# Kernel optimization log

Hardware: AMD Instinct MI355X
Metric: run time of the kernel (lower is better)

Reference implementation:

```python
import jax, jax.numpy as jnp
import numpy as np

B, T, V, E, H = 4096, 128, 30, 256, 128

def setup_inputs() -> dict:
    key = jax.random.key(0)
    ks = jax.random.split(key, 12)
    inpt = jax.random.randint(ks[0], (B, T), 0, V, dtype=jnp.int32)
    h0 = jax.random.normal(ks[1], (B, H), dtype=jnp.float32)
    c0 = jax.random.normal(ks[2], (B, H), dtype=jnp.float32)
    mask_Y = jnp.ones((B, T), dtype=jnp.float32)
    s_e = 1.0
    s_l = 1.0 / np.sqrt(H)
    s_i = 1.0 / np.sqrt(E)
    emb = jax.random.normal(ks[3], (V, E), dtype=jnp.float32) * s_e
    W_ih = jax.random.normal(ks[4], (4 * H, E), dtype=jnp.float32) * s_i
    b_ih = jax.random.normal(ks[5], (4 * H,), dtype=jnp.float32) * s_i
    W_hh = jax.random.normal(ks[6], (4 * H, H), dtype=jnp.float32) * s_l
    b_hh = jax.random.normal(ks[7], (4 * H,), dtype=jnp.float32) * s_l
    W_lin = jax.random.normal(ks[8], (V, H), dtype=jnp.float32) * s_l
    b_lin = jax.random.normal(ks[9], (V,), dtype=jnp.float32) * s_l
    return {"inpt": inpt, "h0": h0, "c0": c0, "mask_Y": mask_Y, "beta": 1,
            "emb": emb, "W_ih": W_ih, "b_ih": b_ih, "W_hh": W_hh,
            "b_hh": b_hh, "W_lin": W_lin, "b_lin": b_lin}


def reference(inpt, h0, c0, mask_Y, beta, emb, W_ih, b_ih, W_hh, b_hh, W_lin, b_lin):
    # beta == 1 -> teacher forcing every step (u <= beta always), as in source.
    t_max = inpt.shape[1]
    # input tokens fed at steps t=0..t_max-2 are inpt[:, 0:t_max-1]
    x_emb = emb[inpt[:, :t_max - 1]]          # [B, T-1, E]
    xs = (jnp.swapaxes(x_emb, 0, 1),           # [T-1, B, E]
          inpt[:, 1:].T,                       # [T-1, B] true labels
          mask_Y[:, :t_max - 1].T)             # [T-1, B]

    def step(carry, xs_t):
        h, c = carry
        x, y, m = xs_t
        gates = x @ W_ih.T + b_ih + h @ W_hh.T + b_hh   # [B, 4H]
        i, f, g, o = jnp.split(gates, 4, axis=1)
        c2 = jax.nn.sigmoid(f) * c + jax.nn.sigmoid(i) * jnp.tanh(g)
        h2 = jax.nn.sigmoid(o) * jnp.tanh(c2)
        # -log(softmax(logits))[y] == -log_softmax(logits)[y]
        logp = jax.nn.log_softmax(h2 @ W_lin.T + b_lin, axis=1)  # [B, V]
        ce = -jnp.take_along_axis(logp, y[:, None], axis=1)[:, 0]
        return (h2, c2), jnp.sum(ce * m)

    _, step_losses = jax.lax.scan(step, (h0, c0), xs)
    return jnp.sum(step_losses) / jnp.sum(mask_Y)
```

## Files before the change

### kernel.cpp

```cpp
#include <hip/hip_runtime.h>


typedef __bf16 bf16x8 __attribute__((ext_vector_type(8)));
typedef float  f32x4  __attribute__((ext_vector_type(4)));

namespace {
constexpr int Bn = 4096, Tn = 128, Vn = 30, En = 256, Hn = 128, Gn = 512;
constexpr int WS_LOSS  = 0;
constexpr int WS_MASK  = 1;
constexpr int WS_CNT   = 2;
constexpr int WS_XPROJ = 16;
constexpr int WS_WF_F  = WS_XPROJ + Vn * Gn;
}

__device__ __forceinline__ float fexp2(float x) { return __builtin_amdgcn_exp2f(x); }
__device__ __forceinline__ float frcp(float x)  { return __builtin_amdgcn_rcpf(x); }
__device__ __forceinline__ float sigf(float x)  { return frcp(1.f + fexp2(x * -1.44269504f)); }
__device__ __forceinline__ float tanh_(float x) { return 1.f - 2.f * frcp(fexp2(x * 2.88539008f) + 1.f); }

__global__ void k_setup(const float* __restrict__ emb, const float* __restrict__ W_ih,
                        const float* __restrict__ b_ih, const float* __restrict__ b_hh,
                        const float* __restrict__ W_hh, const float* __restrict__ W_lin,
                        float* __restrict__ ws) {
  const int bid = blockIdx.x, tid = threadIdx.x;
  if (bid < 60) {
    __shared__ __align__(16) float es[En];
    int v = bid >> 1;
    int j = ((bid & 1) << 8) + tid;
    es[tid] = emb[v * En + tid];
    __syncthreads();
    float a = b_ih[j] + b_hh[j];
    const float* wr = W_ih + j * En;
#pragma unroll 4
    for (int e = 0; e < En; e += 4) {
      float4 w = *(const float4*)(wr + e);
      float4 x = *(const float4*)(es + e);
      a += x.x * w.x + x.y * w.y + x.z * w.z + x.w * w.w;
    }
    ws[WS_XPROJ + v * Gn + (j & 127) * 4 + (j >> 7)] = a;
  } else if (bid < 92) {
    int fid = (bid - 60) * 256 + tid;
    int l = fid & 63, kt = (fid >> 6) & 3, g = (fid >> 8) & 3, w = fid >> 10;
    int n  = (g * 8 + w) * 16 + (l & 15);
    int k0 = kt * 32 + (l >> 4) * 8;
    const float* src = W_hh + n * Hn + k0;
    union { __bf16 h[8]; uint4 u; } pk;
#pragma unroll
    for (int j = 0; j < 8; ++j) pk.h[j] = (__bf16)src[j];
    __bf16* wf = (__bf16*)(ws + WS_WF_F);
    *(uint4*)(wf + fid * 8) = pk.u;
  } else {
    int fid = (bid - 92) * 256 + tid;
    if (fid < 3) ws[fid] = 0.f;
    int l = fid & 63, kt = (fid >> 6) & 3, n = fid >> 8;
    int col = n * 16 + (l & 15);
    int k0  = kt * 32 + (l >> 4) * 8;
    union { __bf16 h[8]; uint4 u; } pk;
#pragma unroll
    for (int j = 0; j < 8; ++j)
      pk.h[j] = (col < Vn) ? (__bf16)W_lin[col * Hn + k0 + j] : (__bf16)0.f;
    __bf16* wf = (__bf16*)(ws + WS_WF_F);
    *(uint4*)(wf + 65536 + fid * 8) = pk.u;
  }
}

__global__ __launch_bounds__(576, 1) void k_main(
    const int* __restrict__ inpt, const float* __restrict__ h0,
    const float* __restrict__ c0, const float* __restrict__ maskY,
    const float* __restrict__ b_lin, float* __restrict__ ws,
    float* __restrict__ out) {
  __shared__ __align__(16) __bf16 hbuf[2][16][136];
  __shared__ int   tokL[16 * 129];
  __shared__ float maskL[16 * 132];
  __shared__ __align__(16) float logits[16 * 36];
  __shared__ float red[2];

  const float4* X4 = (const float4*)(ws + WS_XPROJ);
  const __bf16* wf = (const __bf16*)(ws + WS_WF_F);
  const __bf16* wlf = wf + 65536;

  const int tid = threadIdx.x;
  const int w = tid >> 6, l = tid & 63, quad = l >> 4, lc = l & 15;
  const int row0 = blockIdx.x * 16;
  const int kh = w * 16 + lc;

  for (int idx = tid; idx < 16 * Tn; idx += 576) {
    int r = idx >> 7, t = idx & 127;
    tokL[r * 129 + t]  = inpt[(row0 + r) * Tn + t];
    maskL[r * 132 + t] = maskY[(row0 + r) * Tn + t];
  }
  for (int idx = tid; idx < 16 * Hn; idx += 576) {
    int r = idx >> 7, k = idx & 127;
    hbuf[0][r][k] = (__bf16)h0[(row0 + r) * Hn + k];
  }

  bf16x8 wreg[4][4];
  float  creg[4];
  float  bias0 = 0.f, bias1 = 0.f, mloc = 0.f;
  if (w < 8) {
#pragma unroll
    for (int g = 0; g < 4; ++g)
#pragma unroll
      for (int kt = 0; kt < 4; ++kt)
        wreg[g][kt] = __builtin_bit_cast(
            bf16x8, *(const uint4*)(wf + (((w * 4 + g) * 4 + kt) * 64 + l) * 8));
#pragma unroll
    for (int p = 0; p < 4; ++p)
      creg[p] = c0[(row0 + quad * 4 + p) * Hn + kh];
    if (w == 7) {
      float s = 0.f;
      const float4* m4 = (const float4*)(maskY + row0 * Tn);
#pragma unroll
      for (int i = 0; i < 8; ++i) s += m4[l + i * 64].x + m4[l + i * 64].y +
                                       m4[l + i * 64].z + m4[l + i * 64].w;
      mloc = s;
    }
  } else {
#pragma unroll
    for (int n = 0; n < 2; ++n)
#pragma unroll
      for (int kt = 0; kt < 4; ++kt)
        wreg[n][kt] = __builtin_bit_cast(
            bf16x8, *(const uint4*)(wlf + ((n * 4 + kt) * 64 + l) * 8));
    bias0 = b_lin[lc];
    bias1 = (lc < Vn - 16) ? b_lin[lc + 16] : -1e30f;
  }
  float ce_acc = 0.f;
  __syncthreads();

  float4 xv[4];
  if (w < 8) {
#pragma unroll
    for (int p = 0; p < 4; ++p)
      xv[p] = X4[tokL[(quad * 4 + p) * 129] * 128 + kh];
  }

  for (int t = 0; t < Tn; ++t) {
    const int par = t & 1;
    const __bf16* hc = &hbuf[par][0][0];
    __bf16*       hn = &hbuf[par ^ 1][0][0];

    if (w < 8) {
      if (t < Tn - 1) {
        bf16x8 af[4];
#pragma unroll
        for (int kt = 0; kt < 4; ++kt)
          af[kt] = __builtin_bit_cast(
              bf16x8, *(const uint4*)(hc + lc * 136 + kt * 32 + quad * 8));

        int tk[4];
#pragma unroll
        for (int p = 0; p < 4; ++p) tk[p] = tokL[(quad * 4 + p) * 129 + t + 1];

        f32x4 acc[4];
#pragma unroll
        for (int p = 0; p < 4; ++p) {
          acc[0][p] = xv[p].x; acc[1][p] = xv[p].y;
          acc[2][p] = xv[p].z; acc[3][p] = xv[p].w;
        }
#pragma unroll
        for (int g = 0; g < 4; ++g)
#pragma unroll
          for (int kt = 0; kt < 4; ++kt)
            acc[g] = __builtin_amdgcn_mfma_f32_16x16x32_bf16(af[kt], wreg[g][kt], acc[g], 0, 0, 0);

        float4 xn[4];
#pragma unroll
        for (int p = 0; p < 4; ++p) xn[p] = X4[tk[p] * 128 + kh];

#pragma unroll
        for (int p = 0; p < 4; ++p) {
          float c2 = sigf(acc[1][p]) * creg[p] + sigf(acc[0][p]) * tanh_(acc[2][p]);
          float h2 = sigf(acc[3][p]) * tanh_(c2);
          creg[p] = c2;
          hn[(quad * 4 + p) * 136 + kh] = (__bf16)h2;
          xv[p] = xn[p];
        }
      }
    } else if (t >= 1) {
      bf16x8 af[4];
#pragma unroll
      for (int kt = 0; kt < 4; ++kt)
        af[kt] = __builtin_bit_cast(
            bf16x8, *(const uint4*)(hc + lc * 136 + kt * 32 + quad * 8));
      f32x4 lacc[2] = {{bias0, bias0, bias0, bias0}, {bias1, bias1, bias1, bias1}};
#pragma unroll
      for (int kt = 0; kt < 4; ++kt) {
        lacc[0] = __builtin_amdgcn_mfma_f32_16x16x32_bf16(af[kt], wreg[0][kt], lacc[0], 0, 0, 0);
        lacc[1] = __builtin_amdgcn_mfma_f32_16x16x32_bf16(af[kt], wreg[1][kt], lacc[1], 0, 0, 0);
      }
#pragma unroll
      for (int p = 0; p < 4; ++p) {
        logits[(quad * 4 + p) * 36 + lc]      = lacc[0][p];
        logits[(quad * 4 + p) * 36 + 16 + lc] = lacc[1][p];
      }
      int row = l >> 2, j = l & 3;
      float4 v0 = *(const float4*)(logits + row * 36 + j * 8);
      float4 v1 = *(const float4*)(logits + row * 36 + j * 8 + 4);
      float m = fmaxf(fmaxf(fmaxf(v0.x, v0.y), fmaxf(v0.z, v0.w)),
                      fmaxf(fmaxf(v1.x, v1.y), fmaxf(v1.z, v1.w)));
      m = fmaxf(m, __shfl_xor(m, 1));
      m = fmaxf(m, __shfl_xor(m, 2));
      float e = fexp2((v0.x - m) * 1.44269504f) + fexp2((v0.y - m) * 1.44269504f) +
                fexp2((v0.z - m) * 1.44269504f) + fexp2((v0.w - m) * 1.44269504f) +
                fexp2((v1.x - m) * 1.44269504f) + fexp2((v1.y - m) * 1.44269504f) +
                fexp2((v1.z - m) * 1.44269504f) + fexp2((v1.w - m) * 1.44269504f);
      e += __shfl_xor(e, 1);
      e += __shfl_xor(e, 2);
      if (j == 0) {
        int   y  = tokL[row * 129 + t];
        float ly = logits[row * 36 + y];
        float ce = (m + __logf(e)) - ly;
        ce_acc += ce * maskL[row * 132 + t - 1];
      }
    }
    __syncthreads();
  }

  if (w == 7) {
#pragma unroll
    for (int off = 32; off > 0; off >>= 1) mloc += __shfl_down(mloc, off);
    if (l == 0) red[0] = mloc;
  }
  __syncthreads();
  if (w == 8) {
#pragma unroll
    for (int off = 32; off > 0; off >>= 1) ce_acc += __shfl_down(ce_acc, off);
    if (l == 0) {
      atomicAdd(ws + WS_LOSS, ce_acc);
      atomicAdd(ws + WS_MASK, red[0]);
      __threadfence();
      unsigned old = atomicAdd((unsigned*)(ws + WS_CNT), 1u);
      if (old == 255) {
        float lv = atomicAdd(ws + WS_LOSS, 0.f);
        float mv = atomicAdd(ws + WS_MASK, 0.f);
        out[0] = lv / mv;
      }
    }
  }
}

extern "C" void kernel_launch(void* const* d_in, const int* in_sizes, int n_in,
                              void* d_out, int out_size, void* d_ws, size_t ws_size,
                              hipStream_t stream) {
  const int*   inpt  = (const int*)  d_in[0];
  const float* h0    = (const float*)d_in[1];
  const float* c0    = (const float*)d_in[2];
  const float* maskY = (const float*)d_in[3];
  const float* emb   = (const float*)d_in[5];
  const float* W_ih  = (const float*)d_in[6];
  const float* b_ih  = (const float*)d_in[7];
  const float* W_hh  = (const float*)d_in[8];
  const float* b_hh  = (const float*)d_in[9];
  const float* W_lin = (const float*)d_in[10];
  const float* b_lin = (const float*)d_in[11];
  float* ws  = (float*)d_ws;
  float* out = (float*)d_out;

  hipLaunchKernelGGL(k_setup, dim3(94),  dim3(256), 0, stream,
                     emb, W_ih, b_ih, b_hh, W_hh, W_lin, ws);
  hipLaunchKernelGGL(k_main,  dim3(256), dim3(576), 0, stream,
                     inpt, h0, c0, maskY, b_lin, ws, out);
}
```

Baseline: 229.1 us.

## Split batch into 8-row blocks to double grid size across CUs

Each block now handles 8 batch rows instead of 16, so the grid doubles to 512 blocks. The top 8 rows of the 16-row MFMA tile are zero-padded, and gate values are redistributed with shuffles so every lane does elementwise LSTM work for 2 rows instead of 4. Launch bounds are relaxed to allow several blocks per CU. The aim is to spread the sequential recurrence over more CUs and shorten each step's elementwise tail, at the cost of half-wasted MFMA work and extra shuffles.

```diff
diff --git a/kernel.cpp b/kernel.cpp
--- a/kernel.cpp
+++ b/kernel.cpp
@@ -11,6 +11,7 @@
 constexpr int WS_CNT   = 2;
 constexpr int WS_XPROJ = 16;
 constexpr int WS_WF_F  = WS_XPROJ + Vn * Gn;
+constexpr int NBLK = 512;
 }
 
 __device__ __forceinline__ float fexp2(float x) { return __builtin_amdgcn_exp2f(x); }
@@ -64,38 +65,43 @@
   }
 }
 
-__global__ __launch_bounds__(576, 1) void k_main(
+__global__ __launch_bounds__(576, 4) void k_main(
     const int* __restrict__ inpt, const float* __restrict__ h0,
     const float* __restrict__ c0, const float* __restrict__ maskY,
     const float* __restrict__ b_lin, float* __restrict__ ws,
     float* __restrict__ out) {
   __shared__ __align__(16) __bf16 hbuf[2][16][136];
-  __shared__ int   tokL[16 * 129];
-  __shared__ float maskL[16 * 132];
-  __shared__ __align__(16) float logits[16 * 36];
+  __shared__ int   tokL[8 * 129];
+  __shared__ float maskL[8 * 132];
+  __shared__ __align__(16) float logits[8 * 36];
   __shared__ float red[2];
 
-  const float4* X4 = (const float4*)(ws + WS_XPROJ);
-  const __bf16* wf = (const __bf16*)(ws + WS_WF_F);
+  const float4* X4  = (const float4*)(ws + WS_XPROJ);
+  const __bf16* wf  = (const __bf16*)(ws + WS_WF_F);
   const __bf16* wlf = wf + 65536;
 
   const int tid = threadIdx.x;
   const int w = tid >> 6, l = tid & 63, quad = l >> 4, lc = l & 15;
-  const int row0 = blockIdx.x * 16;
+  const int row0 = blockIdx.x * 8;
   const int kh = w * 16 + lc;
-
-  for (int idx = tid; idx < 16 * Tn; idx += 576) {
+  const int prow0 = (quad < 2) ? quad * 4 : (quad - 2) * 4 + 2;
+
+  for (int idx = tid; idx < 8 * Tn; idx += 576) {
     int r = idx >> 7, t = idx & 127;
     tokL[r * 129 + t]  = inpt[(row0 + r) * Tn + t];
     maskL[r * 132 + t] = maskY[(row0 + r) * Tn + t];
   }
-  for (int idx = tid; idx < 16 * Hn; idx += 576) {
+  for (int idx = tid; idx < 8 * Hn; idx += 576) {
     int r = idx >> 7, k = idx & 127;
     hbuf[0][r][k] = (__bf16)h0[(row0 + r) * Hn + k];
   }
+  for (int idx = tid; idx < 2 * 8 * 136; idx += 576) {
+    int pr = idx / (8 * 136), rem = idx - pr * (8 * 136);
+    hbuf[pr][8 + rem / 136][rem % 136] = (__bf16)0.f;
+  }
 
   bf16x8 wreg[4][4];
-  float  creg[4];
+  float  creg[2];
   float  bias0 = 0.f, bias1 = 0.f, mloc = 0.f;
   if (w < 8) {
 #pragma unroll
@@ -105,13 +111,13 @@
         wreg[g][kt] = __builtin_bit_cast(
             bf16x8, *(const uint4*)(wf + (((w * 4 + g) * 4 + kt) * 64 + l) * 8));
 #pragma unroll
-    for (int p = 0; p < 4; ++p)
-      creg[p] = c0[(row0 + quad * 4 + p) * Hn + kh];
+    for (int p = 0; p < 2; ++p)
+      creg[p] = c0[(row0 + prow0 + p) * Hn + kh];
     if (w == 7) {
       float s = 0.f;
       const float4* m4 = (const float4*)(maskY + row0 * Tn);
 #pragma unroll
-      for (int i = 0; i < 8; ++i) s += m4[l + i * 64].x + m4[l + i * 64].y +
+      for (int i = 0; i < 4; ++i) s += m4[l + i * 64].x + m4[l + i * 64].y +
                                        m4[l + i * 64].z + m4[l + i * 64].w;
       mloc = s;
     }
@@ -129,7 +135,7 @@
   __syncthreads();
 
   float4 xv[4];
-  if (w < 8) {
+  if (w < 8 && quad < 2) {
 #pragma unroll
     for (int p = 0; p < 4; ++p)
       xv[p] = X4[tokL[(quad * 4 + p) * 129] * 128 + kh];
@@ -149,14 +155,16 @@
               bf16x8, *(const uint4*)(hc + lc * 136 + kt * 32 + quad * 8));
 
         int tk[4];
-#pragma unroll
-        for (int p = 0; p < 4; ++p) tk[p] = tokL[(quad * 4 + p) * 129 + t + 1];
+        if (quad < 2) {
+#pragma unroll
+          for (int p = 0; p < 4; ++p) tk[p] = tokL[(quad * 4 + p) * 129 + t + 1];
+        }
 
         f32x4 acc[4];
 #pragma unroll
         for (int p = 0; p < 4; ++p) {
-          acc[0][p] = xv[p].x; acc[1][p] = xv[p].y;
-          acc[2][p] = xv[p].z; acc[3][p] = xv[p].w;
+          float4 x = (quad < 2) ? xv[p] : float4{0.f, 0.f, 0.f, 0.f};
+          acc[0][p] = x.x; acc[1][p] = x.y; acc[2][p] = x.z; acc[3][p] = x.w;
         }
 #pragma unroll
         for (int g = 0; g < 4; ++g)
@@ -165,17 +173,31 @@
             acc[g] = __builtin_amdgcn_mfma_f32_16x16x32_bf16(af[kt], wreg[g][kt], acc[g], 0, 0, 0);
 
         float4 xn[4];
-#pragma unroll
-        for (int p = 0; p < 4; ++p) xn[p] = X4[tk[p] * 128 + kh];
-
-#pragma unroll
-        for (int p = 0; p < 4; ++p) {
-          float c2 = sigf(acc[1][p]) * creg[p] + sigf(acc[0][p]) * tanh_(acc[2][p]);
-          float h2 = sigf(acc[3][p]) * tanh_(c2);
+        if (quad < 2) {
+#pragma unroll
+          for (int p = 0; p < 4; ++p) xn[p] = X4[tk[p] * 128 + kh];
+        }
+
+        float mv[4][2];
+#pragma unroll
+        for (int g = 0; g < 4; ++g)
+#pragma unroll
+          for (int pp = 0; pp < 2; ++pp)
+            mv[g][pp] = __shfl(acc[g][2 + pp], l & 31);
+
+#pragma unroll
+        for (int p = 0; p < 2; ++p) {
+          float gi = (quad < 2) ? acc[0][p] : mv[0][p];
+          float gf = (quad < 2) ? acc[1][p] : mv[1][p];
+          float gg = (quad < 2) ? acc[2][p] : mv[2][p];
+          float go = (quad < 2) ? acc[3][p] : mv[3][p];
+          float c2 = sigf(gf) * creg[p] + sigf(gi) * tanh_(gg);
+          float h2 = sigf(go) * tanh_(c2);
           creg[p] = c2;
-          hn[(quad * 4 + p) * 136 + kh] = (__bf16)h2;
-          xv[p] = xn[p];
-        }
+          hn[(prow0 + p) * 136 + kh] = (__bf16)h2;
+        }
+#pragma unroll
+        for (int p = 0; p < 4; ++p) xv[p] = xn[p];
       }
     } else if (t >= 1) {
       bf16x8 af[4];
@@ -189,29 +211,33 @@
         lacc[0] = __builtin_amdgcn_mfma_f32_16x16x32_bf16(af[kt], wreg[0][kt], lacc[0], 0, 0, 0);
         lacc[1] = __builtin_amdgcn_mfma_f32_16x16x32_bf16(af[kt], wreg[1][kt], lacc[1], 0, 0, 0);
       }
-#pragma unroll
-      for (int p = 0; p < 4; ++p) {
-        logits[(quad * 4 + p) * 36 + lc]      = lacc[0][p];
-        logits[(quad * 4 + p) * 36 + 16 + lc] = lacc[1][p];
-      }
-      int row = l >> 2, j = l & 3;
-      float4 v0 = *(const float4*)(logits + row * 36 + j * 8);
-      float4 v1 = *(const float4*)(logits + row * 36 + j * 8 + 4);
-      float m = fmaxf(fmaxf(fmaxf(v0.x, v0.y), fmaxf(v0.z, v0.w)),
-                      fmaxf(fmaxf(v1.x, v1.y), fmaxf(v1.z, v1.w)));
-      m = fmaxf(m, __shfl_xor(m, 1));
-      m = fmaxf(m, __shfl_xor(m, 2));
-      float e = fexp2((v0.x - m) * 1.44269504f) + fexp2((v0.y - m) * 1.44269504f) +
-                fexp2((v0.z - m) * 1.44269504f) + fexp2((v0.w - m) * 1.44269504f) +
-                fexp2((v1.x - m) * 1.44269504f) + fexp2((v1.y - m) * 1.44269504f) +
-                fexp2((v1.z - m) * 1.44269504f) + fexp2((v1.w - m) * 1.44269504f);
-      e += __shfl_xor(e, 1);
-      e += __shfl_xor(e, 2);
-      if (j == 0) {
-        int   y  = tokL[row * 129 + t];
-        float ly = logits[row * 36 + y];
-        float ce = (m + __logf(e)) - ly;
-        ce_acc += ce * maskL[row * 132 + t - 1];
+      if (quad < 2) {
+#pragma unroll
+        for (int p = 0; p < 4; ++p) {
+          logits[(quad * 4 + p) * 36 + lc]      = lacc[0][p];
+          logits[(quad * 4 + p) * 36 + 16 + lc] = lacc[1][p];
+        }
+      }
+      if (l < 32) {
+        int row = l >> 2, j = l & 3;
+        float4 v0 = *(const float4*)(logits + row * 36 + j * 8);
+        float4 v1 = *(const float4*)(logits + row * 36 + j * 8 + 4);
+        float m = fmaxf(fmaxf(fmaxf(v0.x, v0.y), fmaxf(v0.z, v0.w)),
+                        fmaxf(fmaxf(v1.x, v1.y), fmaxf(v1.z, v1.w)));
+        m = fmaxf(m, __shfl_xor(m, 1));
+        m = fmaxf(m, __shfl_xor(m, 2));
+        float e = fexp2((v0.x - m) * 1.44269504f) + fexp2((v0.y - m) * 1.44269504f) +
+                  fexp2((v0.z - m) * 1.44269504f) + fexp2((v0.w - m) * 1.44269504f) +
+                  fexp2((v1.x - m) * 1.44269504f) + fexp2((v1.y - m) * 1.44269504f) +
+                  fexp2((v1.z - m) * 1.44269504f) + fexp2((v1.w - m) * 1.44269504f);
+        e += __shfl_xor(e, 1);
+        e += __shfl_xor(e, 2);
+        if (j == 0) {
+          int   y  = tokL[row * 129 + t];
+          float ly = logits[row * 36 + y];
+          float ce = (m + __logf(e)) - ly;
+          ce_acc += ce * maskL[row * 132 + t - 1];
+        }
       }
     }
     __syncthreads();
@@ -231,10 +257,10 @@
       atomicAdd(ws + WS_MASK, red[0]);
       __threadfence();
       unsigned old = atomicAdd((unsigned*)(ws + WS_CNT), 1u);
-      if (old == 255) {
+      if (old == NBLK - 1) {
         float lv = atomicAdd(ws + WS_LOSS, 0.f);
-        float mv = atomicAdd(ws + WS_MASK, 0.f);
-        out[0] = lv / mv;
+        float mv2 = atomicAdd(ws + WS_MASK, 0.f);
+        out[0] = lv / mv2;
       }
     }
   }
@@ -257,8 +283,8 @@
   float* ws  = (float*)d_ws;
   float* out = (float*)d_out;
 
-  hipLaunchKernelGGL(k_setup, dim3(94),  dim3(256), 0, stream,
+  hipLaunchKernelGGL(k_setup, dim3(94),   dim3(256), 0, stream,
                      emb, W_ih, b_ih, b_hh, W_hh, W_lin, ws);
-  hipLaunchKernelGGL(k_main,  dim3(256), dim3(576), 0, stream,
+  hipLaunchKernelGGL(k_main,  dim3(NBLK), dim3(576), 0, stream,
                      inpt, h0, c0, maskY, b_lin, ws, out);
 }
```

Result: slower. 496.9 us (+116.9%).
